# Optimization experiments

Measured on AMD Instinct MI355X. Metric: run time of the kernel, lower is better.

## Reference

```python
import jax, jax.numpy as jnp
import numpy as np

N, N_SPINS, N_HIDDEN = 8192, 1024, 1024


def setup_inputs() -> dict:
    key = jax.random.key(0)
    ks = jax.random.split(key, 6)
    s_in = 1.0 / np.sqrt(N_SPINS)
    s_h = 1.0 / np.sqrt(N_HIDDEN)
    return {
        "x": jax.random.normal(ks[0], (N, N_SPINS), dtype=jnp.float32),
        "W_in": jax.random.normal(ks[1], (N_HIDDEN, N_SPINS), dtype=jnp.float32) * s_in,
        "b_in": jax.random.normal(ks[2], (N_HIDDEN,), dtype=jnp.float32) * s_in,
        "Wq": jax.random.normal(ks[3], (N_HIDDEN, N_HIDDEN), dtype=jnp.float32) * s_h,
        "Wk": jax.random.normal(ks[4], (N_HIDDEN, N_HIDDEN), dtype=jnp.float32) * s_h,
        "Wv": jax.random.normal(ks[5], (N_HIDDEN, N_HIDDEN), dtype=jnp.float32) * s_h,
    }


def reference(x, W_in, b_in, Wq, Wk, Wv):
    # embedding: Linear(n_spins, n_hidden)  -> h: [N, H]
    h = x @ W_in.T + b_in
    q = h @ Wq.T                      # [N, H]
    k = h @ Wk.T                      # [N, H]
    v = h @ Wv.T                      # [N, H]
    scores = (q @ k.T) * 0.25         # [N, N], scale 1/4 as in source
    attn = jax.nn.softmax(scores, axis=0)  # softmax over dim=0 (columns)
    out = attn @ v                    # [N, H]
    # log(cosh(z)) = |z| + log1p(exp(-2|z|)) - log(2), numerically stable
    a = jnp.abs(out)
    logcosh = a + jnp.log1p(jnp.exp(-2.0 * a)) - jnp.log(jnp.asarray(2.0, out.dtype))
    return jnp.sum(logcosh, axis=-1)  # [N]
```

## Files before the change

### kernel.cpp

```cpp
#include <hip/hip_runtime.h>
#include <hip/hip_bf16.h>
#include <cstdint>
#include <cstddef>

#define NTOK 8192
#define NHID 1024

typedef __attribute__((ext_vector_type(8))) __bf16 bf16x8;
typedef __attribute__((ext_vector_type(4))) float f32x4;

__device__ __forceinline__ unsigned short f2bf(float f) {
    union { float f; unsigned u; } v; v.f = f;
    unsigned r = v.u + 0x7FFF + ((v.u >> 16) & 1);
    return (unsigned short)(r >> 16);
}

__device__ __forceinline__ float bf2f(unsigned short u) {
    union { unsigned u; float f; } v; v.u = ((unsigned)u) << 16;
    return v.f;
}

__device__ __forceinline__ void async_copy16(const void* gsrc, void* ldsdst) {
    __builtin_amdgcn_global_load_lds(
        (const __attribute__((address_space(1))) unsigned int*)gsrc,
        (__attribute__((address_space(3))) unsigned int*)ldsdst,
        16, 0, 0);
}

template <int EPI, bool SWAP>
__global__ __launch_bounds__(512, 2) void gemm_bt2(
    const unsigned short* __restrict__ A,
    const unsigned short* __restrict__ B,
    void* __restrict__ C,
    const float* __restrict__ bias,
    float* __restrict__ zsum,
    float scale, int M, int N, int K, int lda, int ldb)
{
    __shared__ __attribute__((aligned(16))) unsigned short lds[3][24576];

    const int tid  = threadIdx.x;
    const int wave = tid >> 6;
    const int lane = tid & 63;
    const int bm = (SWAP ? blockIdx.x : blockIdx.y) * 256;
    const int bn = (SWAP ? blockIdx.y : blockIdx.x) * 128;
    const size_t ldaz = (size_t)lda;
    const size_t ldbz = (size_t)ldb;

    const int srow = lane >> 3;
    const int scol = ((lane & 7) ^ srow) * 8;
    const unsigned short* Ag[4];
    const unsigned short* Bg[2];
    int Aoff[4], Boff[2];
#pragma unroll
    for (int t = 0; t < 4; ++t) {
        int r = (wave * 4 + t) * 8 + srow;
        Ag[t] = A + (size_t)(bm + r) * ldaz + scol;
        Aoff[t] = (wave * 4 + t) * 512;
    }
#pragma unroll
    for (int t = 0; t < 2; ++t) {
        int r = (wave * 2 + t) * 8 + srow;
        Bg[t] = B + (size_t)(bn + r) * ldbz + scol;
        Boff[t] = 16384 + (wave * 2 + t) * 512;
    }

    const int wm = (wave >> 1) * 64;
    const int wn = (wave & 1) * 64;
    const int fr = lane & 15;
    const int frl = fr & 7;
    const int q = lane >> 4;

    f32x4 acc[4][4] = {};

    const int nt = K >> 6;

    auto stage = [&](int s) {
        unsigned short* base = &lds[s][0];
#pragma unroll
        for (int t = 0; t < 4; ++t) { async_copy16(Ag[t], base + Aoff[t]); Ag[t] += 64; }
#pragma unroll
        for (int t = 0; t < 2; ++t) { async_copy16(Bg[t], base + Boff[t]); Bg[t] += 64; }
    };

    stage(0);
    stage(1);
    asm volatile("s_waitcnt vmcnt(6)" ::: "memory");
    __builtin_amdgcn_s_barrier();

    int cb = 0;
    int sb = 2;
    for (int t = 0; t < nt; ++t) {
        if (t + 2 < nt) {
            stage(sb);
            sb = (sb == 2) ? 0 : sb + 1;
        }
        const unsigned short* As = &lds[cb][0];
        const unsigned short* Bs = &lds[cb][16384];
#pragma unroll
        for (int ks = 0; ks < 2; ++ks) {
            const int pc = ((ks * 4 + q) ^ frl) * 8;
            bf16x8 a[4], b[4];
#pragma unroll
            for (int i = 0; i < 4; ++i) {
                a[i] = *(const bf16x8*)&As[(wm + i * 16 + fr) * 64 + pc];
                b[i] = *(const bf16x8*)&Bs[(wn + i * 16 + fr) * 64 + pc];
            }
            __builtin_amdgcn_s_setprio(1);
#pragma unroll
            for (int i = 0; i < 4; ++i)
#pragma unroll
                for (int j = 0; j < 4; ++j)
                    acc[i][j] = __builtin_amdgcn_mfma_f32_16x16x32_bf16(
                        a[i], b[j], acc[i][j], 0, 0, 0);
            __builtin_amdgcn_s_setprio(0);
        }
        if (t < nt - 1) {
            if (t < nt - 2) asm volatile("s_waitcnt vmcnt(6)" ::: "memory");
            else            asm volatile("s_waitcnt vmcnt(0)" ::: "memory");
            __builtin_amdgcn_s_barrier();
            cb = (cb == 2) ? 0 : cb + 1;
        }
    }

    const int erow = q * 4;
#pragma unroll
    for (int j = 0; j < 4; ++j) {
        const int gcol = bn + wn + j * 16 + fr;
        const float bv = (EPI == 1 && bias) ? bias[gcol] : 0.0f;
        float colsum = 0.0f;
#pragma unroll
        for (int i = 0; i < 4; ++i) {
            const int grow0 = bm + wm + i * 16 + erow;
#pragma unroll
            for (int r = 0; r < 4; ++r) {
                float v;
                if (EPI == 2) {
                    v = __expf(fmaf(acc[i][j][r], scale, -64.0f));
                    colsum += v;
                } else {
                    v = acc[i][j][r] * scale + bv;
                }
                size_t idx = (size_t)(grow0 + r) * N + gcol;
                if (EPI == 0) ((float*)C)[idx] = v;
                else          ((unsigned short*)C)[idx] = f2bf(v);
            }
        }
        if (EPI == 2) {
            colsum += __shfl_xor(colsum, 16, 64);
            colsum += __shfl_xor(colsum, 32, 64);
            if (q == 0) atomicAdd(&zsum[gcol], colsum);
        }
    }
}

__global__ void cvt_all(const float4* __restrict__ x,
                        const float4* __restrict__ w0,
                        const float4* __restrict__ w1,
                        const float4* __restrict__ w2,
                        const float4* __restrict__ w3,
                        ushort4* __restrict__ xb,
                        ushort4* __restrict__ wdst,
                        float4* __restrict__ pz4,
                        int n4x, int n4w)
{
    int i = blockIdx.x * blockDim.x + threadIdx.x;
    int n4 = n4x + 4 * n4w;
    if (i >= n4) {
        int zi = i - n4;
        if (zi < 2048) pz4[zi] = make_float4(0.f, 0.f, 0.f, 0.f);
        return;
    }
    float4 f;
    ushort4* dst;
    if (i < n4x) {
        f = x[i]; dst = xb + i;
    } else {
        int r = i - n4x;
        int seg = r / n4w, off = r % n4w;
        const float4* src = (seg == 0) ? w0 : (seg == 1) ? w1 : (seg == 2) ? w2 : w3;
        f = src[off]; dst = wdst + r;
    }
    ushort4 o;
    o.x = f2bf(f.x); o.y = f2bf(f.y); o.z = f2bf(f.z); o.w = f2bf(f.w);
    *dst = o;
}

__global__ __launch_bounds__(256) void transpose_scale(
    const unsigned short* __restrict__ v,
    const float* __restrict__ z,
    unsigned short* __restrict__ vt)
{
    __shared__ float lds[64 * 65];
    const int tid = threadIdx.x;
    const int j0 = blockIdx.x * 64;
    const int h0 = blockIdx.y * 64;
    const int c = tid & 63;
    const int r0 = tid >> 6;
#pragma unroll
    for (int it = 0; it < 16; ++it) {
        int r = it * 4 + r0;
        lds[r * 65 + c] = bf2f(v[(size_t)(j0 + r) * 3072 + h0 + c]);
    }
    __syncthreads();
    const float rz = 1.0f / z[j0 + c];
#pragma unroll
    for (int it = 0; it < 16; ++it) {
        int r = it * 4 + r0;
        vt[(size_t)(h0 + r) * NTOK + j0 + c] = f2bf(lds[c * 65 + r] * rz);
    }
}

__global__ void logcosh_rowsum(const ushort4* __restrict__ O4,
                               float* __restrict__ out)
{
    const float LN2 = 0.69314718055994531f;
    int row = blockIdx.x;
    ushort4 u = O4[(size_t)row * 256 + threadIdx.x];
    float s = 0.0f, a;
    a = fabsf(bf2f(u.x)); s += a + log1pf(__expf(-2.0f * a));
    a = fabsf(bf2f(u.y)); s += a + log1pf(__expf(-2.0f * a));
    a = fabsf(bf2f(u.z)); s += a + log1pf(__expf(-2.0f * a));
    a = fabsf(bf2f(u.w)); s += a + log1pf(__expf(-2.0f * a));
    s -= 4.0f * LN2;
    for (int off = 32; off; off >>= 1) s += __shfl_down(s, off, 64);
    __shared__ float red[4];
    if ((threadIdx.x & 63) == 0) red[threadIdx.x >> 6] = s;
    __syncthreads();
    if (threadIdx.x == 0) out[row] = red[0] + red[1] + red[2] + red[3];
}

extern "C" void kernel_launch(void* const* d_in, const int* in_sizes, int n_in,
                              void* d_out, int out_size, void* d_ws, size_t ws_size,
                              hipStream_t stream)
{
    (void)in_sizes; (void)n_in; (void)out_size; (void)ws_size;

    const float* x    = (const float*)d_in[0];
    const float* W_in = (const float*)d_in[1];
    const float* b_in = (const float*)d_in[2];
    const float* Wq   = (const float*)d_in[3];
    const float* Wk   = (const float*)d_in[4];
    const float* Wv   = (const float*)d_in[5];
    float* out = (float*)d_out;

    char* w = (char*)d_ws;
    const size_t MiB = 1024 * 1024;
    unsigned short* Pb     = (unsigned short*)(w);
    unsigned short* qkv    = (unsigned short*)(w + 128 * MiB);
    unsigned short* xb     = (unsigned short*)(w + 128 * MiB);
    unsigned short* outb   = (unsigned short*)(w + 128 * MiB);
    unsigned short* hb     = (unsigned short*)(w + 176 * MiB);
    unsigned short* vtb    = (unsigned short*)(w + 176 * MiB);
    unsigned short* wib    = (unsigned short*)(w + 192 * MiB);
    unsigned short* wqkvb  = (unsigned short*)(w + 194 * MiB);
    float*          pz     = (float*)         (w + 200 * MiB);

    {
        int n4x = NTOK * NHID / 4;
        int n4w = NHID * NHID / 4;
        int n4  = n4x + 4 * n4w;
        cvt_all<<<n4 / 256 + 8, 256, 0, stream>>>(
            (const float4*)x, (const float4*)W_in, (const float4*)Wq,
            (const float4*)Wk, (const float4*)Wv,
            (ushort4*)xb, (ushort4*)wib, (float4*)pz, n4x, n4w);
    }

    dim3 gNH(NHID / 128, NTOK / 256);
    gemm_bt2<1, false><<<gNH, 512, 0, stream>>>(
        xb, wib, hb, b_in, nullptr, 1.0f, NTOK, NHID, NHID, NHID, NHID);

    dim3 gQKV(3 * NHID / 128, NTOK / 256);
    gemm_bt2<1, false><<<gQKV, 512, 0, stream>>>(
        hb, wqkvb, qkv, nullptr, nullptr, 1.0f, NTOK, 3 * NHID, NHID, NHID, NHID);

    dim3 gS(NTOK / 128, NTOK / 256);
    gemm_bt2<2, false><<<gS, 512, 0, stream>>>(
        qkv, qkv + NHID, Pb, nullptr, pz, 0.25f, NTOK, NTOK, NHID,
        3 * NHID, 3 * NHID);

    dim3 gT(NTOK / 64, NHID / 64);
    transpose_scale<<<gT, 256, 0, stream>>>(qkv + 2 * NHID, pz, vtb);

    dim3 gO(NTOK / 256, NHID / 128);
    gemm_bt2<1, true><<<gO, 512, 0, stream>>>(
        Pb, vtb, outb, nullptr, nullptr, 1.0f, NTOK, NHID, NTOK, NTOK, NTOK);

    logcosh_rowsum<<<NTOK, 256, 0, stream>>>((const ushort4*)outb, out);
}
```

Measured before the change: 483.5 us.

## Interleave async prefetch issue with MFMA sub-steps using ping-pong barriers

```diff
diff --git a/kernel.cpp b/kernel.cpp
--- a/kernel.cpp
+++ b/kernel.cpp
@@ -28,7 +28,7 @@
 }
 
 template <int EPI, bool SWAP>
-__global__ __launch_bounds__(512, 2) void gemm_bt2(
+__global__ __launch_bounds__(512, 2) void gemm_bt3(
     const unsigned short* __restrict__ A,
     const unsigned short* __restrict__ B,
     void* __restrict__ C,
@@ -74,37 +74,43 @@
 
     const int nt = K >> 6;
 
-    auto stage = [&](int s) {
-        unsigned short* base = &lds[s][0];
-#pragma unroll
-        for (int t = 0; t < 4; ++t) { async_copy16(Ag[t], base + Aoff[t]); Ag[t] += 64; }
-#pragma unroll
-        for (int t = 0; t < 2; ++t) { async_copy16(Bg[t], base + Boff[t]); Bg[t] += 64; }
-    };
-
-    stage(0);
-    stage(1);
-    asm volatile("s_waitcnt vmcnt(6)" ::: "memory");
-    __builtin_amdgcn_s_barrier();
+    {
+        unsigned short* b0 = &lds[0][0];
+        unsigned short* b1 = &lds[1][0];
+#pragma unroll
+        for (int u = 0; u < 4; ++u) { async_copy16(Ag[u], b0 + Aoff[u]); Ag[u] += 64; }
+#pragma unroll
+        for (int u = 0; u < 2; ++u) { async_copy16(Bg[u], b0 + Boff[u]); Bg[u] += 64; }
+#pragma unroll
+        for (int u = 0; u < 4; ++u) { async_copy16(Ag[u], b1 + Aoff[u]); Ag[u] += 64; }
+#pragma unroll
+        for (int u = 0; u < 2; ++u) { async_copy16(Bg[u], b1 + Boff[u]); Bg[u] += 64; }
+        asm volatile("s_waitcnt vmcnt(6)" ::: "memory");
+        __builtin_amdgcn_s_barrier();
+    }
 
     int cb = 0;
     int sb = 2;
     for (int t = 0; t < nt; ++t) {
-        if (t + 2 < nt) {
-            stage(sb);
-            sb = (sb == 2) ? 0 : sb + 1;
-        }
         const unsigned short* As = &lds[cb][0];
         const unsigned short* Bs = &lds[cb][16384];
-#pragma unroll
-        for (int ks = 0; ks < 2; ++ks) {
-            const int pc = ((ks * 4 + q) ^ frl) * 8;
+        unsigned short* Sb = &lds[sb][0];
+        const bool pf = (t + 2 < nt);
+
+        {
+            const int pc = (q ^ frl) * 8;
             bf16x8 a[4], b[4];
 #pragma unroll
             for (int i = 0; i < 4; ++i) {
                 a[i] = *(const bf16x8*)&As[(wm + i * 16 + fr) * 64 + pc];
                 b[i] = *(const bf16x8*)&Bs[(wn + i * 16 + fr) * 64 + pc];
             }
+            if (pf) {
+#pragma unroll
+                for (int u = 0; u < 4; ++u) { async_copy16(Ag[u], Sb + Aoff[u]); Ag[u] += 64; }
+            }
+            __builtin_amdgcn_s_barrier();
+            asm volatile("s_waitcnt lgkmcnt(0)" ::: "memory");
             __builtin_amdgcn_s_setprio(1);
 #pragma unroll
             for (int i = 0; i < 4; ++i)
@@ -113,13 +119,38 @@
                     acc[i][j] = __builtin_amdgcn_mfma_f32_16x16x32_bf16(
                         a[i], b[j], acc[i][j], 0, 0, 0);
             __builtin_amdgcn_s_setprio(0);
+            __builtin_amdgcn_s_barrier();
         }
-        if (t < nt - 1) {
-            if (t < nt - 2) asm volatile("s_waitcnt vmcnt(6)" ::: "memory");
-            else            asm volatile("s_waitcnt vmcnt(0)" ::: "memory");
+
+        {
+            const int pc = ((4 + q) ^ frl) * 8;
+            bf16x8 a[4], b[4];
+#pragma unroll
+            for (int i = 0; i < 4; ++i) {
+                a[i] = *(const bf16x8*)&As[(wm + i * 16 + fr) * 64 + pc];
+                b[i] = *(const bf16x8*)&Bs[(wn + i * 16 + fr) * 64 + pc];
+            }
+            if (pf) {
+#pragma unroll
+                for (int u = 0; u < 2; ++u) { async_copy16(Bg[u], Sb + Boff[u]); Bg[u] += 64; }
+            }
             __builtin_amdgcn_s_barrier();
-            cb = (cb == 2) ? 0 : cb + 1;
+            asm volatile("s_waitcnt lgkmcnt(0)" ::: "memory");
+            __builtin_amdgcn_s_setprio(1);
+#pragma unroll
+            for (int i = 0; i < 4; ++i)
+#pragma unroll
+                for (int j = 0; j < 4; ++j)
+                    acc[i][j] = __builtin_amdgcn_mfma_f32_16x16x32_bf16(
+                        a[i], b[j], acc[i][j], 0, 0, 0);
+            __builtin_amdgcn_s_setprio(0);
+            if (t < nt - 2)       asm volatile("s_waitcnt vmcnt(6)" ::: "memory");
+            else if (t == nt - 2) asm volatile("s_waitcnt vmcnt(0)" ::: "memory");
+            __builtin_amdgcn_s_barrier();
         }
+
+        if (pf) sb = (sb == 2) ? 0 : sb + 1;
+        cb = (cb == 2) ? 0 : cb + 1;
     }
 
     const int erow = q * 4;
@@ -266,15 +297,15 @@
     }
 
     dim3 gNH(NHID / 128, NTOK / 256);
-    gemm_bt2<1, false><<<gNH, 512, 0, stream>>>(
+    gemm_bt3<1, false><<<gNH, 512, 0, stream>>>(
         xb, wib, hb, b_in, nullptr, 1.0f, NTOK, NHID, NHID, NHID, NHID);
 
     dim3 gQKV(3 * NHID / 128, NTOK / 256);
-    gemm_bt2<1, false><<<gQKV, 512, 0, stream>>>(
+    gemm_bt3<1, false><<<gQKV, 512, 0, stream>>>(
         hb, wqkvb, qkv, nullptr, nullptr, 1.0f, NTOK, 3 * NHID, NHID, NHID, NHID);
 
     dim3 gS(NTOK / 128, NTOK / 256);
-    gemm_bt2<2, false><<<gS, 512, 0, stream>>>(
+    gemm_bt3<2, false><<<gS, 512, 0, stream>>>(
         qkv, qkv + NHID, Pb, nullptr, pz, 0.25f, NTOK, NTOK, NHID,
         3 * NHID, 3 * NHID);
 
@@ -282,7 +313,7 @@
     transpose_scale<<<gT, 256, 0, stream>>>(qkv + 2 * NHID, pz, vtb);
 
     dim3 gO(NTOK / 256, NHID / 128);
-    gemm_bt2<1, true><<<gO, 512, 0, stream>>>(
+    gemm_bt3<1, true><<<gO, 512, 0, stream>>>(
         Pb, vtb, outb, nullptr, nullptr, 1.0f, NTOK, NHID, NTOK, NTOK, NTOK);
 
     logcosh_rowsum<<<NTOK, 256, 0, stream>>>((const ushort4*)outb, out);
```

Result: no change. 477.4 us (-1.3%).
